# Kernel tuning notes

Hardware: AMD Instinct MI355X
Metric: run time of the kernel (lower is better)

The kernel has to match this reference:

```python
import jax, jax.numpy as jnp
import numpy as np

LN_EPS = 1e-5

def _layernorm(x, g, b):
    mu = jnp.mean(x, axis=-1, keepdims=True)
    var = jnp.mean(jnp.square(x - mu), axis=-1, keepdims=True)
    return (x - mu) * jax.lax.rsqrt(var + LN_EPS) * g + b

def setup_inputs() -> dict:
    key = jax.random.key(0)
    ks = jax.random.split(key, 8)
    B, T, C = 4, 2048, 1024
    s = 0.02
    return {
        "x": jax.random.normal(ks[0], (B, T, C), jnp.float32),
        "w_qkv": jax.random.normal(ks[1], (C, 3 * C), jnp.float32) * s,
        "b_qkv": jnp.zeros((3 * C,), jnp.float32),
        "w_out": jax.random.normal(ks[2], (C, C), jnp.float32) * s,
        "b_out": jnp.zeros((C,), jnp.float32),
        "w1": jax.random.normal(ks[3], (C, 4 * C), jnp.float32) * s,
        "b1": jnp.zeros((4 * C,), jnp.float32),
        "w2": jax.random.normal(ks[4], (4 * C, C), jnp.float32) * s,
        "b2": jnp.zeros((C,), jnp.float32),
        "g1": jnp.ones((C,), jnp.float32),
        "be1": jnp.zeros((C,), jnp.float32),
        "g2": jnp.ones((C,), jnp.float32),
        "be2": jnp.zeros((C,), jnp.float32),
        "n_head": 16,
    }

def reference(x, w_qkv, b_qkv, w_out, b_out, w1, b1, w2, b2, g1, be1, g2, be2, n_head):
    B, T, C = x.shape
    H = n_head
    D = C // H
    # --- causal self-attention ---
    qkv = x @ w_qkv + b_qkv                      # [B,T,3C]
    q, k, v = jnp.split(qkv, 3, axis=-1)
    q = q.reshape(B, T, H, D).transpose(0, 2, 1, 3)  # [B,H,T,D]
    k = k.reshape(B, T, H, D).transpose(0, 2, 1, 3)
    v = v.reshape(B, T, H, D).transpose(0, 2, 1, 3)
    attn = jnp.einsum("bhqd,bhkd->bhqk", q, k) * (1.0 / np.sqrt(D))
    causal = jnp.tril(jnp.ones((T, T), bool))
    attn = jnp.where(causal, attn, jnp.float32(-jnp.inf))
    attn = jax.nn.softmax(attn, axis=-1)
    y = jnp.einsum("bhqk,bhkd->bhqd", attn, v)
    y = y.transpose(0, 2, 1, 3).reshape(B, T, C)
    y = y @ w_out + b_out
    # post-norm residual (norm applied to sublayer output)
    x = x + _layernorm(y, g1, be1)
    # --- MLP ---
    h = jax.nn.gelu(x @ w1 + b1, approximate=False)
    h = h @ w2 + b2
    x = x + _layernorm(h, g2, be2)
    return x
```

## Files before the change

### kernel.cpp

```cpp
#include <hip/hip_runtime.h>
#include <hip/hip_bf16.h>

typedef unsigned short ushort_t;
using bf16x8 = __attribute__((ext_vector_type(8))) short;
using f32x4  = __attribute__((ext_vector_type(4))) float;

#define DEV __device__ __forceinline__

DEV unsigned short f2bf(float f) {
    unsigned int u = __builtin_bit_cast(unsigned int, f);
    u = (u + 0x7fffu + ((u >> 16) & 1u)) >> 16;
    return (unsigned short)u;
}

DEV int cvtpk_bf16(float lo, float hi) {
    int r;
    asm("v_cvt_pk_bf16_f32 %0, %1, %2" : "=v"(r) : "v"(lo), "v"(hi));
    return r;
}

DEV void gload16(const unsigned short* g, unsigned short* l) {
    __builtin_amdgcn_global_load_lds(
        (const __attribute__((address_space(1))) void*)g,
        (__attribute__((address_space(3))) void*)l, 16, 0, 0);
}

DEV float gelu_f(float v) {
    float u = v * (0.79788456f + 0.03567741f * v * v);
    float t = __builtin_amdgcn_exp2f(u * 2.88539008f);
    return v * t * __builtin_amdgcn_rcpf(t + 1.0f);
}

__global__ __launch_bounds__(256) void cvtbf_kernel(const float* __restrict__ in,
                                                    unsigned short* __restrict__ out) {
    int i = (blockIdx.x * 256 + threadIdx.x) * 4;
    float4 v = *(const float4*)&in[i];
    out[i + 0] = f2bf(v.x);
    out[i + 1] = f2bf(v.y);
    out[i + 2] = f2bf(v.z);
    out[i + 3] = f2bf(v.w);
}

__global__ __launch_bounds__(256) void transpose_cvt_kernel(const float* __restrict__ in,
                                                            unsigned short* __restrict__ out,
                                                            int R, int C) {
    __shared__ float t[32][33];
    int tx = threadIdx.x, ty = threadIdx.y;
    int c0 = blockIdx.x * 32, r0 = blockIdx.y * 32;
#pragma unroll
    for (int i = 0; i < 4; ++i)
        t[ty + i * 8][tx] = in[(size_t)(r0 + ty + i * 8) * C + c0 + tx];
    __syncthreads();
#pragma unroll
    for (int i = 0; i < 4; ++i)
        out[(size_t)(c0 + ty + i * 8) * R + r0 + tx] = f2bf(t[tx][ty + i * 8]);
}

__global__ __launch_bounds__(256) void vtrans_kernel(const unsigned short* __restrict__ qkvb,
                                                     unsigned short* __restrict__ vtg) {
    __shared__ unsigned short t[64 * 66];
    const int tid = threadIdx.x;
    const int t0 = blockIdx.x * 64;
    const int bh = blockIdx.y;
    const int b = bh >> 4, h = bh & 15;
    const unsigned short* src = qkvb + (size_t)(b * 2048 + t0) * 3072 + 2048 + h * 64;
#pragma unroll
    for (int c = 0; c < 2; ++c) {
        int cid = c * 256 + tid;
        int row = cid >> 3, cc = cid & 7;
        *(int4*)&t[row * 66 + cc * 8] = *(const int4*)&src[(size_t)row * 3072 + cc * 8];
    }
    __syncthreads();
    unsigned short* dst = vtg + (size_t)bh * 64 * 2048 + t0;
#pragma unroll
    for (int c = 0; c < 2; ++c) {
        int cid = c * 256 + tid;
        int d = cid >> 3, cc2 = cid & 7;
        bf16x8 v;
#pragma unroll
        for (int j = 0; j < 8; ++j) v[j] = (short)t[(cc2 * 8 + j) * 66 + d];
        *(bf16x8*)&dst[(size_t)d * 2048 + cc2 * 8] = v;
    }
}

template <int BM, int ACT, int OBF>
__global__ __launch_bounds__(512, 2) void gemm256_kernel(
    const unsigned short* __restrict__ A, const unsigned short* __restrict__ Bt,
    const float* __restrict__ bias, void* __restrict__ out,
    int N, int K, int gridNt) {
    constexpr int MF = BM / 32;
    constexpr int ALD = BM / 64;
    constexpr int NW = ALD / 2 + 2;
    constexpr int LB = (BM == 256) ? 8 : 7;
    __shared__ __align__(16) unsigned short lA[2][BM * 64];
    __shared__ __align__(16) unsigned short lB[2][256 * 64];
    const int tid = threadIdx.x;
    const int lane = tid & 63, wid = tid >> 6;
    const int g = lane >> 4, lr = lane & 15;
    const int wm = wid >> 2, wn = wid & 3;

    const int nwg = gridDim.x, cpx = nwg >> 3, bid = blockIdx.x;
    const int wkid = (bid & 7) * cpx + (bid >> 3);
    const int mt = wkid / gridNt, nt = wkid % gridNt;
    const int m0 = mt * BM, n0 = nt * 256;

    auto stageA = [&](int s, int kt, int bb) {
        int c = s * 512 + tid;
        int row = c & (BM - 1), kb = c >> LB;
        gload16(&A[(size_t)(m0 + row) * K + kt * 64 + kb * 8],
                &lA[bb][(size_t)(s * 512 + (tid & ~63)) * 8]);
    };
    auto stageB = [&](int s, int kt, int bb) {
        int c = s * 512 + tid;
        int row = c & 255, kb = c >> 8;
        gload16(&Bt[(size_t)(n0 + row) * K + kt * 64 + kb * 8],
                &lB[bb][(size_t)(s * 512 + (tid & ~63)) * 8]);
    };
    auto stageKh = [&](int half, int kt, int bb) {
        if constexpr (BM == 256) {
            stageA(half * 2 + 0, kt, bb);
            stageA(half * 2 + 1, kt, bb);
            stageB(half * 2 + 0, kt, bb);
            stageB(half * 2 + 1, kt, bb);
        } else {
            stageA(half, kt, bb);
            stageB(half * 2 + 0, kt, bb);
            stageB(half * 2 + 1, kt, bb);
        }
    };

    f32x4 acc[MF][4] = {};
    bf16x8 af[MF];
    bf16x8 bfr[4];

    const int nkt = K >> 6;
    stageKh(0, 0, 0);
    stageKh(1, 0, 0);

    for (int kt = 0; kt < nkt; ++kt) {
        const int b = kt & 1;
        const bool more = (kt + 1 < nkt);
#pragma unroll
        for (int ks = 0; ks < 2; ++ks) {
            if (ks == 1 && !more)
                asm volatile("s_waitcnt vmcnt(0)" ::: "memory");
            else if constexpr (BM == 256)
                asm volatile("s_waitcnt vmcnt(4)" ::: "memory");
            else
                asm volatile("s_waitcnt vmcnt(3)" ::: "memory");
            __builtin_amdgcn_s_barrier();
            asm volatile("" ::: "memory");
#pragma unroll
            for (int mf = 0; mf < MF; ++mf) {
                int c = (ks * 4 + g) * BM + wm * (BM / 2) + mf * 16 + lr;
                af[mf] = *(const bf16x8*)&lA[b][(size_t)c * 8];
            }
#pragma unroll
            for (int nf = 0; nf < 4; ++nf) {
                int c = (ks * 4 + g) * 256 + wn * 64 + nf * 16 + lr;
                bfr[nf] = *(const bf16x8*)&lB[b][(size_t)c * 8];
            }
            if (more) stageKh(ks, kt + 1, b ^ 1);
            __builtin_amdgcn_s_setprio(1);
#pragma unroll
            for (int mf = 0; mf < MF; ++mf)
#pragma unroll
                for (int nf = 0; nf < 4; ++nf)
                    acc[mf][nf] = __builtin_amdgcn_mfma_f32_16x16x32_bf16(
                        af[mf], bfr[nf], acc[mf][nf], 0, 0, 0);
            __builtin_amdgcn_s_setprio(0);
        }
    }

#pragma unroll
    for (int mf = 0; mf < MF; ++mf) {
#pragma unroll
        for (int nf = 0; nf < 4; ++nf) {
            int col = n0 + wn * 64 + nf * 16 + lr;
            float bv = bias[col];
#pragma unroll
            for (int r = 0; r < 4; ++r) {
                int row = m0 + wm * (BM / 2) + mf * 16 + g * 4 + r;
                float v = acc[mf][nf][r] + bv;
                if (ACT == 1) v = gelu_f(v);
                if (OBF)
                    ((unsigned short*)out)[(size_t)row * N + col] = f2bf(v);
                else
                    ((float*)out)[(size_t)row * N + col] = v;
            }
        }
    }
}

__global__ __launch_bounds__(256) void attn_kernel(const unsigned short* __restrict__ qkv,
                                                   const unsigned short* __restrict__ vtg,
                                                   unsigned short* __restrict__ y) {
    __shared__ unsigned short Kl[2][4096];
    __shared__ unsigned short Vl[2][4096];
    const int tid = threadIdx.x, lane = tid & 63, w = tid >> 6;
    const int g = lane >> 4, lr = lane & 15;
    const int p = blockIdx.x, h = blockIdx.y, b = blockIdx.z;
    const int bh = b * 16 + h;
    const size_t rs3 = 3072;
    const unsigned short* qbase = qkv + (size_t)b * 2048 * rs3 + h * 64;
    const unsigned short* kbase = qbase + 1024;
    const unsigned short* vbase = vtg + (size_t)bh * 64 * 2048;

    int ksoff[2], vsoff[2], ldoff[2];
#pragma unroll
    for (int c = 0; c < 2; ++c) {
        int row = w * 16 + c * 8 + (lane >> 3);
        int ccs = (lane & 7) ^ (row & 7) ^ (row >> 3);
        ksoff[c] = row * 3072 + ccs * 8;
        vsoff[c] = row * 2048 + ccs * 8;
        ldoff[c] = (w * 16 + c * 8) * 64;
    }

    const int idxP0 = 4 * (32 * (g & 1) + lr);
    const int idxP1 = idxP0 + 64;
    int idxA[4];
#pragma unroll
    for (int r = 0; r < 4; ++r) idxA[r] = 4 * (g * 20 + r);
    const bool ghigh = (g >> 1) != 0;
    const float qscale = 0.125f * 1.44269504089f;

    auto process = [&](int J) {
        const int q0w = J * 128 + w * 32;
        const int ktend = 2 * J + 2;
#pragma unroll
        for (int c = 0; c < 2; ++c) {
            gload16(&kbase[ksoff[c]], &Kl[0][ldoff[c]]);
            gload16(&vbase[vsoff[c]], &Vl[0][ldoff[c]]);
        }
        int qf[2][2][4];
#pragma unroll
        for (int sub = 0; sub < 2; ++sub)
#pragma unroll
            for (int f = 0; f < 2; ++f) {
                int4 v = *(const int4*)&qbase[(size_t)(q0w + sub * 16 + lr) * rs3 + f * 32 + g * 8];
                int vv[4] = {v.x, v.y, v.z, v.w};
#pragma unroll
                for (int i = 0; i < 4; ++i) {
                    unsigned int u = (unsigned int)vv[i];
                    float lo = __builtin_bit_cast(float, u << 16) * qscale;
                    float hi = __builtin_bit_cast(float, u & 0xffff0000u) * qscale;
                    qf[sub][f][i] = cvtpk_bf16(lo, hi);
                }
            }

        f32x4 O[2][4] = {};
        float m_[2] = {-3.0e38f, -3.0e38f}, l_[2] = {0.f, 0.f};

        int buf = 0;
        for (int kt = 0; kt < ktend; ++kt) {
            asm volatile("s_waitcnt vmcnt(0)" ::: "memory");
            __builtin_amdgcn_s_barrier();
            asm volatile("" ::: "memory");
            if (kt + 1 < ktend) {
#pragma unroll
                for (int c = 0; c < 2; ++c) {
                    gload16(&kbase[(size_t)(kt + 1) * 64 * 3072 + ksoff[c]], &Kl[buf ^ 1][ldoff[c]]);
                    gload16(&vbase[vsoff[c] + (kt + 1) * 64], &Vl[buf ^ 1][ldoff[c]]);
                }
            }
            const unsigned short* Kc = Kl[buf];
            const unsigned short* Vc = Vl[buf];

            const bool act0 = (kt * 64) <= (q0w + 15);
            const bool act1 = (kt * 64) <= (q0w + 31);

            f32x4 s0[4], s1[4];
#pragma unroll
            for (int st = 0; st < 4; ++st) {
                int rbase = (st * 16 + lr) * 64;
                int sw = (lr & 7) ^ (st * 2 + (lr >> 3));
                bf16x8 kf0 = *(const bf16x8*)&Kc[rbase + ((g ^ sw) * 8)];
                bf16x8 kf1 = *(const bf16x8*)&Kc[rbase + (((4 + g) ^ sw) * 8)];
                if (act0) {
                    f32x4 a = {};
                    a = __builtin_amdgcn_mfma_f32_16x16x32_bf16(kf0, *(const bf16x8*)&qf[0][0], a, 0, 0, 0);
                    a = __builtin_amdgcn_mfma_f32_16x16x32_bf16(kf1, *(const bf16x8*)&qf[0][1], a, 0, 0, 0);
                    s0[st] = a;
                }
                if (act1) {
                    f32x4 a = {};
                    a = __builtin_amdgcn_mfma_f32_16x16x32_bf16(kf0, *(const bf16x8*)&qf[1][0], a, 0, 0, 0);
                    a = __builtin_amdgcn_mfma_f32_16x16x32_bf16(kf1, *(const bf16x8*)&qf[1][1], a, 0, 0, 0);
                    s1[st] = a;
                }
            }

            int wt0[2][4], wt1[2][4];
#pragma unroll
            for (int sub = 0; sub < 2; ++sub) {
                if (sub == 0 && !act0) continue;
                if (sub == 1 && !act1) continue;
                f32x4* s = (sub == 0) ? s0 : s1;
                const int qmin = q0w + sub * 16;
                if (kt * 64 + 63 > qmin) {
                    int qv = qmin + lr;
#pragma unroll
                    for (int st = 0; st < 4; ++st) {
                        int keyb = kt * 64 + st * 16 + g * 4;
#pragma unroll
                        for (int r = 0; r < 4; ++r)
                            if (keyb + r > qv) s[st][r] = -3.0e38f;
                    }
                }
                float mx = fmaxf(fmaxf(s[0][0], s[0][1]), fmaxf(s[0][2], s[0][3]));
#pragma unroll
                for (int st = 1; st < 4; ++st)
                    mx = fmaxf(mx, fmaxf(fmaxf(s[st][0], s[st][1]), fmaxf(s[st][2], s[st][3])));
                mx = fmaxf(mx, __shfl_xor(mx, 16));
                mx = fmaxf(mx, __shfl_xor(mx, 32));
                float mold = m_[sub];
                float mnew = fmaxf(mold, mx);
                float alpha = __builtin_amdgcn_exp2f(mold - mnew);
                m_[sub] = mnew;
                float rs = 0.f;
#pragma unroll
                for (int st = 0; st < 4; ++st)
#pragma unroll
                    for (int r = 0; r < 4; ++r) {
                        float pp = __builtin_amdgcn_exp2f(s[st][r] - mnew);
                        s[st][r] = pp;
                        rs += pp;
                    }
                rs += __shfl_xor(rs, 16);
                rs += __shfl_xor(rs, 32);
                l_[sub] = l_[sub] * alpha + rs;
                int av = __builtin_bit_cast(int, alpha);
                f32x4* Os = O[sub];
#pragma unroll
                for (int r = 0; r < 4; ++r) {
                    float ar = __builtin_bit_cast(float, __builtin_amdgcn_ds_bpermute(idxA[r], av));
#pragma unroll
                    for (int dt = 0; dt < 4; ++dt) Os[dt][r] *= ar;
                }
                int ws_[4][2];
#pragma unroll
                for (int st = 0; st < 4; ++st) {
                    ws_[st][0] = cvtpk_bf16(s[st][0], s[st][1]);
                    ws_[st][1] = cvtpk_bf16(s[st][2], s[st][3]);
                }
                int(*wt)[4] = (sub == 0) ? wt0 : wt1;
#pragma unroll
                for (int ks = 0; ks < 2; ++ks)
#pragma unroll
                    for (int hp = 0; hp < 4; ++hp) {
                        int idx = (hp < 2) ? idxP0 : idxP1;
                        int v0 = __builtin_amdgcn_ds_bpermute(idx, ws_[2 * ks][hp & 1]);
                        int v1 = __builtin_amdgcn_ds_bpermute(idx, ws_[2 * ks + 1][hp & 1]);
                        wt[ks][hp] = ghigh ? v1 : v0;
                    }
            }

#pragma unroll
            for (int ks = 0; ks < 2; ++ks) {
                bf16x8 pa0 = *(const bf16x8*)&wt0[ks][0];
                bf16x8 pa1 = *(const bf16x8*)&wt1[ks][0];
#pragma unroll
                for (int dt = 0; dt < 4; ++dt) {
                    int d = dt * 16 + lr;
                    int xv = (ks * 4 + g) ^ (lr & 7) ^ (dt * 2 + (lr >> 3));
                    bf16x8 vf = *(const bf16x8*)&Vc[d * 64 + xv * 8];
                    if (act0) O[0][dt] = __builtin_amdgcn_mfma_f32_16x16x32_bf16(pa0, vf, O[0][dt], 0, 0, 0);
                    if (act1) O[1][dt] = __builtin_amdgcn_mfma_f32_16x16x32_bf16(pa1, vf, O[1][dt], 0, 0, 0);
                }
            }
            buf ^= 1;
        }

#pragma unroll
        for (int sub = 0; sub < 2; ++sub) {
            int lv = __builtin_bit_cast(int, l_[sub]);
#pragma unroll
            for (int r = 0; r < 4; ++r) {
                float lval = __builtin_bit_cast(float, __builtin_amdgcn_ds_bpermute(idxA[r], lv));
                float inv = __builtin_amdgcn_rcpf(lval);
                int q = q0w + sub * 16 + g * 4 + r;
#pragma unroll
                for (int dt = 0; dt < 4; ++dt)
                    y[(size_t)(b * 2048 + q) * 1024 + h * 64 + dt * 16 + lr] =
                        f2bf(O[sub][dt][r] * inv);
            }
        }
    };

    process(15 - p);
    __syncthreads();
    process(p);
}

template <int WRITE_BF>
__global__ __launch_bounds__(256) void ln_kernel(const float* __restrict__ base,
                                                 const float* __restrict__ delta,
                                                 const float* __restrict__ gw,
                                                 const float* __restrict__ bw,
                                                 float* __restrict__ outf,
                                                 unsigned short* __restrict__ outb) {
    const int row = blockIdx.x;
    const int tid = threadIdx.x;
    const float* d = delta + (size_t)row * 1024;
    const float* bs = base + (size_t)row * 1024;
    float4 x = *(const float4*)&d[tid * 4];
    float s = x.x + x.y + x.z + x.w;
    float s2 = x.x * x.x + x.y * x.y + x.z * x.z + x.w * x.w;
#pragma unroll
    for (int off = 1; off < 64; off <<= 1) {
        s += __shfl_xor(s, off);
        s2 += __shfl_xor(s2, off);
    }
    __shared__ float red[8];
    if ((tid & 63) == 0) {
        red[tid >> 6] = s;
        red[4 + (tid >> 6)] = s2;
    }
    __syncthreads();
    s = red[0] + red[1] + red[2] + red[3];
    s2 = red[4] + red[5] + red[6] + red[7];
    float mu = s * (1.f / 1024.f);
    float var = s2 * (1.f / 1024.f) - mu * mu;
    float rsig = rsqrtf(var + 1e-5f);
    float4 bb = *(const float4*)&bs[tid * 4];
    float4 gv = *(const float4*)&gw[tid * 4];
    float4 bv = *(const float4*)&bw[tid * 4];
    float4 o;
    o.x = bb.x + (x.x - mu) * rsig * gv.x + bv.x;
    o.y = bb.y + (x.y - mu) * rsig * gv.y + bv.y;
    o.z = bb.z + (x.z - mu) * rsig * gv.z + bv.z;
    o.w = bb.w + (x.w - mu) * rsig * gv.w + bv.w;
    *(float4*)&outf[(size_t)row * 1024 + tid * 4] = o;
    if (WRITE_BF) {
        unsigned short* ob = outb + (size_t)row * 1024 + tid * 4;
        ob[0] = f2bf(o.x);
        ob[1] = f2bf(o.y);
        ob[2] = f2bf(o.z);
        ob[3] = f2bf(o.w);
    }
}

extern "C" void kernel_launch(void* const* d_in, const int* in_sizes, int n_in,
                              void* d_out, int out_size, void* d_ws, size_t ws_size,
                              hipStream_t stream) {
    const float* x = (const float*)d_in[0];
    const float* w_qkv = (const float*)d_in[1];
    const float* b_qkv = (const float*)d_in[2];
    const float* w_out = (const float*)d_in[3];
    const float* b_out = (const float*)d_in[4];
    const float* w1 = (const float*)d_in[5];
    const float* b1 = (const float*)d_in[6];
    const float* w2 = (const float*)d_in[7];
    const float* b2 = (const float*)d_in[8];
    const float* g1 = (const float*)d_in[9];
    const float* be1 = (const float*)d_in[10];
    const float* g2 = (const float*)d_in[11];
    const float* be2 = (const float*)d_in[12];

    const size_t MB = 1ull << 20;
    if (ws_size < 184 * MB) return;
    char* ws = (char*)d_ws;
    unsigned short* xb    = (unsigned short*)(ws + 0);
    unsigned short* vtg   = (unsigned short*)(ws + 0);
    unsigned short* wqkvt = (unsigned short*)(ws + 16 * MB);
    unsigned short* qkvb  = (unsigned short*)(ws + 22 * MB);
    unsigned short* hb    = (unsigned short*)(ws + 0);
    unsigned short* woutt = (unsigned short*)(ws + 70 * MB);
    unsigned short* yb    = (unsigned short*)(ws + 72 * MB);
    float*          attnp = (float*)(ws + 88 * MB);
    float*          ff    = (float*)(ws + 88 * MB);
    float*          x2f   = (float*)(ws + 120 * MB);
    unsigned short* x2b   = (unsigned short*)(ws + 152 * MB);
    unsigned short* w1t   = (unsigned short*)(ws + 168 * MB);
    unsigned short* w2t   = (unsigned short*)(ws + 176 * MB);

    cvtbf_kernel<<<8192, 256, 0, stream>>>(x, xb);
    transpose_cvt_kernel<<<dim3(96, 32), dim3(32, 8), 0, stream>>>(w_qkv, wqkvt, 1024, 3072);
    transpose_cvt_kernel<<<dim3(32, 32), dim3(32, 8), 0, stream>>>(w_out, woutt, 1024, 1024);
    transpose_cvt_kernel<<<dim3(128, 32), dim3(32, 8), 0, stream>>>(w1, w1t, 1024, 4096);
    transpose_cvt_kernel<<<dim3(32, 128), dim3(32, 8), 0, stream>>>(w2, w2t, 4096, 1024);
    gemm256_kernel<256, 0, 1><<<384, 512, 0, stream>>>(xb, wqkvt, b_qkv, qkvb, 3072, 1024, 12);
    vtrans_kernel<<<dim3(32, 64), 256, 0, stream>>>(qkvb, vtg);
    attn_kernel<<<dim3(8, 16, 4), 256, 0, stream>>>(qkvb, vtg, yb);
    gemm256_kernel<128, 0, 0><<<256, 512, 0, stream>>>(yb, woutt, b_out, attnp, 1024, 1024, 4);
    ln_kernel<1><<<8192, 256, 0, stream>>>(x, attnp, g1, be1, x2f, x2b);
    gemm256_kernel<256, 1, 1><<<512, 512, 0, stream>>>(x2b, w1t, b1, hb, 4096, 1024, 16);
    gemm256_kernel<128, 0, 0><<<256, 512, 0, stream>>>(hb, w2t, b2, ff, 1024, 4096, 4);
    ln_kernel<0><<<8192, 256, 0, stream>>>(x2f, ff, g2, be2, (float*)d_out, nullptr);
}
```

Measured before the change: 511.6 us.

## Shrink GEMM tiles to 128x128 and widen attention KV tiles with lazy rescaling

Replaces the 256-wide, 512-thread GEMM with a single 128x128, 256-thread kernel and raises the grid sizes to match, so more workgroups are in flight but each one reuses less data. The attention kernel now loads 128-key K/V tiles, remaps blocks so heads are grouped per XCD, and drops the per-subtile causal activity checks. It also skips the online-softmax rescale unless the running max grows past a threshold. Larger tiles mean fewer loop iterations and barriers, but more wasted masked work on the diagonal and more register pressure.

```diff
diff --git a/kernel.cpp b/kernel.cpp
--- a/kernel.cpp
+++ b/kernel.cpp
@@ -83,87 +83,73 @@
     }
 }
 
-template <int BM, int ACT, int OBF>
-__global__ __launch_bounds__(512, 2) void gemm256_kernel(
+template <int ACT, int OBF>
+__global__ __launch_bounds__(256, 2) void gemm_kernel(
     const unsigned short* __restrict__ A, const unsigned short* __restrict__ Bt,
     const float* __restrict__ bias, void* __restrict__ out,
     int N, int K, int gridNt) {
-    constexpr int MF = BM / 32;
-    constexpr int ALD = BM / 64;
-    constexpr int NW = ALD / 2 + 2;
-    constexpr int LB = (BM == 256) ? 8 : 7;
-    __shared__ __align__(16) unsigned short lA[2][BM * 64];
-    __shared__ __align__(16) unsigned short lB[2][256 * 64];
+    __shared__ __align__(16) unsigned short lA[2][128 * 64];
+    __shared__ __align__(16) unsigned short lB[2][128 * 64];
     const int tid = threadIdx.x;
     const int lane = tid & 63, wid = tid >> 6;
     const int g = lane >> 4, lr = lane & 15;
-    const int wm = wid >> 2, wn = wid & 3;
+    const int wm = wid >> 1, wn = wid & 1;
 
     const int nwg = gridDim.x, cpx = nwg >> 3, bid = blockIdx.x;
     const int wkid = (bid & 7) * cpx + (bid >> 3);
     const int mt = wkid / gridNt, nt = wkid % gridNt;
-    const int m0 = mt * BM, n0 = nt * 256;
+    const int m0 = mt * 128, n0 = nt * 128;
 
     auto stageA = [&](int s, int kt, int bb) {
-        int c = s * 512 + tid;
-        int row = c & (BM - 1), kb = c >> LB;
+        int c = s * 256 + tid;
+        int row = c & 127, kb = c >> 7;
         gload16(&A[(size_t)(m0 + row) * K + kt * 64 + kb * 8],
-                &lA[bb][(size_t)(s * 512 + (tid & ~63)) * 8]);
+                &lA[bb][(size_t)(s * 256 + (tid & ~63)) * 8]);
     };
     auto stageB = [&](int s, int kt, int bb) {
-        int c = s * 512 + tid;
-        int row = c & 255, kb = c >> 8;
+        int c = s * 256 + tid;
+        int row = c & 127, kb = c >> 7;
         gload16(&Bt[(size_t)(n0 + row) * K + kt * 64 + kb * 8],
-                &lB[bb][(size_t)(s * 512 + (tid & ~63)) * 8]);
+                &lB[bb][(size_t)(s * 256 + (tid & ~63)) * 8]);
     };
-    auto stageKh = [&](int half, int kt, int bb) {
-        if constexpr (BM == 256) {
-            stageA(half * 2 + 0, kt, bb);
-            stageA(half * 2 + 1, kt, bb);
-            stageB(half * 2 + 0, kt, bb);
-            stageB(half * 2 + 1, kt, bb);
-        } else {
-            stageA(half, kt, bb);
-            stageB(half * 2 + 0, kt, bb);
-            stageB(half * 2 + 1, kt, bb);
-        }
-    };
-
-    f32x4 acc[MF][4] = {};
-    bf16x8 af[MF];
-    bf16x8 bfr[4];
-
+
+    f32x4 acc[4][4] = {};
     const int nkt = K >> 6;
-    stageKh(0, 0, 0);
-    stageKh(1, 0, 0);
+
+    stageA(0, 0, 0); stageA(1, 0, 0); stageB(0, 0, 0); stageB(1, 0, 0);
+    stageA(2, 0, 0); stageA(3, 0, 0); stageB(2, 0, 0); stageB(3, 0, 0);
 
     for (int kt = 0; kt < nkt; ++kt) {
-        const int b = kt & 1;
+        const int buf = kt & 1;
         const bool more = (kt + 1 < nkt);
 #pragma unroll
         for (int ks = 0; ks < 2; ++ks) {
             if (ks == 1 && !more)
                 asm volatile("s_waitcnt vmcnt(0)" ::: "memory");
-            else if constexpr (BM == 256)
+            else
                 asm volatile("s_waitcnt vmcnt(4)" ::: "memory");
-            else
-                asm volatile("s_waitcnt vmcnt(3)" ::: "memory");
             __builtin_amdgcn_s_barrier();
             asm volatile("" ::: "memory");
-#pragma unroll
-            for (int mf = 0; mf < MF; ++mf) {
-                int c = (ks * 4 + g) * BM + wm * (BM / 2) + mf * 16 + lr;
-                af[mf] = *(const bf16x8*)&lA[b][(size_t)c * 8];
+            bf16x8 af[4], bfr[4];
+#pragma unroll
+            for (int mf = 0; mf < 4; ++mf) {
+                int c = (ks * 4 + g) * 128 + wm * 64 + mf * 16 + lr;
+                af[mf] = *(const bf16x8*)&lA[buf][(size_t)c * 8];
             }
 #pragma unroll
             for (int nf = 0; nf < 4; ++nf) {
-                int c = (ks * 4 + g) * 256 + wn * 64 + nf * 16 + lr;
-                bfr[nf] = *(const bf16x8*)&lB[b][(size_t)c * 8];
-            }
-            if (more) stageKh(ks, kt + 1, b ^ 1);
+                int c = (ks * 4 + g) * 128 + wn * 64 + nf * 16 + lr;
+                bfr[nf] = *(const bf16x8*)&lB[buf][(size_t)c * 8];
+            }
+            if (more) {
+                if (ks == 0) { stageA(0, kt + 1, buf ^ 1); stageA(1, kt + 1, buf ^ 1);
+                               stageB(0, kt + 1, buf ^ 1); stageB(1, kt + 1, buf ^ 1); }
+                else         { stageA(2, kt + 1, buf ^ 1); stageA(3, kt + 1, buf ^ 1);
+                               stageB(2, kt + 1, buf ^ 1); stageB(3, kt + 1, buf ^ 1); }
+            }
             __builtin_amdgcn_s_setprio(1);
 #pragma unroll
-            for (int mf = 0; mf < MF; ++mf)
+            for (int mf = 0; mf < 4; ++mf)
 #pragma unroll
                 for (int nf = 0; nf < 4; ++nf)
                     acc[mf][nf] = __builtin_amdgcn_mfma_f32_16x16x32_bf16(
@@ -173,14 +159,14 @@
     }
 
 #pragma unroll
-    for (int mf = 0; mf < MF; ++mf) {
+    for (int mf = 0; mf < 4; ++mf) {
 #pragma unroll
         for (int nf = 0; nf < 4; ++nf) {
             int col = n0 + wn * 64 + nf * 16 + lr;
             float bv = bias[col];
 #pragma unroll
             for (int r = 0; r < 4; ++r) {
-                int row = m0 + wm * (BM / 2) + mf * 16 + g * 4 + r;
+                int row = m0 + wm * 64 + mf * 16 + g * 4 + r;
                 float v = acc[mf][nf][r] + bv;
                 if (ACT == 1) v = gelu_f(v);
                 if (OBF)
@@ -192,28 +178,32 @@
     }
 }
 
-__global__ __launch_bounds__(256) void attn_kernel(const unsigned short* __restrict__ qkv,
-                                                   const unsigned short* __restrict__ vtg,
-                                                   unsigned short* __restrict__ y) {
-    __shared__ unsigned short Kl[2][4096];
-    __shared__ unsigned short Vl[2][4096];
+__global__ __launch_bounds__(256, 2) void attn_kernel(const unsigned short* __restrict__ qkv,
+                                                      const unsigned short* __restrict__ vtg,
+                                                      unsigned short* __restrict__ y) {
+    __shared__ unsigned short Kl[2][128 * 64];
+    __shared__ unsigned short Vl[2][64 * 128];
     const int tid = threadIdx.x, lane = tid & 63, w = tid >> 6;
     const int g = lane >> 4, lr = lane & 15;
-    const int p = blockIdx.x, h = blockIdx.y, b = blockIdx.z;
-    const int bh = b * 16 + h;
+    const int id = blockIdx.x + 8 * (blockIdx.y + 16 * blockIdx.z);
+    const int xcd = id & 7, wrk = id >> 3;
+    const int bh = xcd * 8 + (wrk & 7);
+    const int p = wrk >> 3;
+    const int b = bh >> 4, h = bh & 15;
     const size_t rs3 = 3072;
     const unsigned short* qbase = qkv + (size_t)b * 2048 * rs3 + h * 64;
     const unsigned short* kbase = qbase + 1024;
     const unsigned short* vbase = vtg + (size_t)bh * 64 * 2048;
 
-    int ksoff[2], vsoff[2], ldoff[2];
-#pragma unroll
-    for (int c = 0; c < 2; ++c) {
-        int row = w * 16 + c * 8 + (lane >> 3);
-        int ccs = (lane & 7) ^ (row & 7) ^ (row >> 3);
-        ksoff[c] = row * 3072 + ccs * 8;
-        vsoff[c] = row * 2048 + ccs * 8;
-        ldoff[c] = (w * 16 + c * 8) * 64;
+    int ksoff[4], vsoff[4], ldoff[4];
+#pragma unroll
+    for (int c = 0; c < 4; ++c) {
+        int cid = c * 256 + tid;
+        int krow = cid >> 3, kcc = cid & 7;
+        ksoff[c] = krow * 3072 + (kcc ^ (krow & 7) ^ ((krow >> 3) & 7)) * 8;
+        int d = cid >> 4, tcs = cid & 15;
+        vsoff[c] = d * 2048 + (tcs ^ ((d & 7) ^ ((d >> 3) & 7))) * 8;
+        ldoff[c] = (c * 256 + (tid & ~63)) * 8;
     }
 
     const int idxP0 = 4 * (32 * (g & 1) + lr);
@@ -226,9 +216,9 @@
 
     auto process = [&](int J) {
         const int q0w = J * 128 + w * 32;
-        const int ktend = 2 * J + 2;
-#pragma unroll
-        for (int c = 0; c < 2; ++c) {
+        const int ktend = J + 1;
+#pragma unroll
+        for (int c = 0; c < 4; ++c) {
             gload16(&kbase[ksoff[c]], &Kl[0][ldoff[c]]);
             gload16(&vbase[vsoff[c]], &Vl[0][ldoff[c]]);
         }
@@ -258,50 +248,41 @@
             asm volatile("" ::: "memory");
             if (kt + 1 < ktend) {
 #pragma unroll
-                for (int c = 0; c < 2; ++c) {
-                    gload16(&kbase[(size_t)(kt + 1) * 64 * 3072 + ksoff[c]], &Kl[buf ^ 1][ldoff[c]]);
-                    gload16(&vbase[vsoff[c] + (kt + 1) * 64], &Vl[buf ^ 1][ldoff[c]]);
+                for (int c = 0; c < 4; ++c) {
+                    gload16(&kbase[(size_t)(kt + 1) * 128 * 3072 + ksoff[c]], &Kl[buf ^ 1][ldoff[c]]);
+                    gload16(&vbase[vsoff[c] + (kt + 1) * 128], &Vl[buf ^ 1][ldoff[c]]);
                 }
             }
             const unsigned short* Kc = Kl[buf];
             const unsigned short* Vc = Vl[buf];
 
-            const bool act0 = (kt * 64) <= (q0w + 15);
-            const bool act1 = (kt * 64) <= (q0w + 31);
-
-            f32x4 s0[4], s1[4];
-#pragma unroll
-            for (int st = 0; st < 4; ++st) {
+            f32x4 s0[8], s1[8];
+#pragma unroll
+            for (int st = 0; st < 8; ++st) {
                 int rbase = (st * 16 + lr) * 64;
-                int sw = (lr & 7) ^ (st * 2 + (lr >> 3));
+                int sw = (lr & 7) ^ ((st * 2 + (lr >> 3)) & 7);
                 bf16x8 kf0 = *(const bf16x8*)&Kc[rbase + ((g ^ sw) * 8)];
                 bf16x8 kf1 = *(const bf16x8*)&Kc[rbase + (((4 + g) ^ sw) * 8)];
-                if (act0) {
-                    f32x4 a = {};
-                    a = __builtin_amdgcn_mfma_f32_16x16x32_bf16(kf0, *(const bf16x8*)&qf[0][0], a, 0, 0, 0);
-                    a = __builtin_amdgcn_mfma_f32_16x16x32_bf16(kf1, *(const bf16x8*)&qf[0][1], a, 0, 0, 0);
-                    s0[st] = a;
-                }
-                if (act1) {
-                    f32x4 a = {};
-                    a = __builtin_amdgcn_mfma_f32_16x16x32_bf16(kf0, *(const bf16x8*)&qf[1][0], a, 0, 0, 0);
-                    a = __builtin_amdgcn_mfma_f32_16x16x32_bf16(kf1, *(const bf16x8*)&qf[1][1], a, 0, 0, 0);
-                    s1[st] = a;
-                }
-            }
-
-            int wt0[2][4], wt1[2][4];
+                f32x4 a = {};
+                a = __builtin_amdgcn_mfma_f32_16x16x32_bf16(kf0, *(const bf16x8*)&qf[0][0], a, 0, 0, 0);
+                a = __builtin_amdgcn_mfma_f32_16x16x32_bf16(kf1, *(const bf16x8*)&qf[0][1], a, 0, 0, 0);
+                s0[st] = a;
+                f32x4 c = {};
+                c = __builtin_amdgcn_mfma_f32_16x16x32_bf16(kf0, *(const bf16x8*)&qf[1][0], c, 0, 0, 0);
+                c = __builtin_amdgcn_mfma_f32_16x16x32_bf16(kf1, *(const bf16x8*)&qf[1][1], c, 0, 0, 0);
+                s1[st] = c;
+            }
+
+            int wt0[4][4], wt1[4][4];
 #pragma unroll
             for (int sub = 0; sub < 2; ++sub) {
-                if (sub == 0 && !act0) continue;
-                if (sub == 1 && !act1) continue;
                 f32x4* s = (sub == 0) ? s0 : s1;
                 const int qmin = q0w + sub * 16;
-                if (kt * 64 + 63 > qmin) {
+                if (kt == J) {
                     int qv = qmin + lr;
 #pragma unroll
-                    for (int st = 0; st < 4; ++st) {
-                        int keyb = kt * 64 + st * 16 + g * 4;
+                    for (int st = 0; st < 8; ++st) {
+                        int keyb = kt * 128 + st * 16 + g * 4;
 #pragma unroll
                         for (int r = 0; r < 4; ++r)
                             if (keyb + r > qv) s[st][r] = -3.0e38f;
@@ -309,43 +290,45 @@
                 }
                 float mx = fmaxf(fmaxf(s[0][0], s[0][1]), fmaxf(s[0][2], s[0][3]));
 #pragma unroll
-                for (int st = 1; st < 4; ++st)
+                for (int st = 1; st < 8; ++st)
                     mx = fmaxf(mx, fmaxf(fmaxf(s[st][0], s[st][1]), fmaxf(s[st][2], s[st][3])));
                 mx = fmaxf(mx, __shfl_xor(mx, 16));
                 mx = fmaxf(mx, __shfl_xor(mx, 32));
-                float mold = m_[sub];
-                float mnew = fmaxf(mold, mx);
-                float alpha = __builtin_amdgcn_exp2f(mold - mnew);
-                m_[sub] = mnew;
+                if (__any(mx - m_[sub] > 11.5f)) {
+                    float mnew = fmaxf(m_[sub], mx);
+                    float alpha = __builtin_amdgcn_exp2f(m_[sub] - mnew);
+                    m_[sub] = mnew;
+                    l_[sub] *= alpha;
+                    int av = __builtin_bit_cast(int, alpha);
+                    f32x4* Os = O[sub];
+#pragma unroll
+                    for (int r = 0; r < 4; ++r) {
+                        float ar = __builtin_bit_cast(float, __builtin_amdgcn_ds_bpermute(idxA[r], av));
+#pragma unroll
+                        for (int dt = 0; dt < 4; ++dt) Os[dt][r] *= ar;
+                    }
+                }
                 float rs = 0.f;
 #pragma unroll
-                for (int st = 0; st < 4; ++st)
+                for (int st = 0; st < 8; ++st)
 #pragma unroll
                     for (int r = 0; r < 4; ++r) {
-                        float pp = __builtin_amdgcn_exp2f(s[st][r] - mnew);
+                        float pp = __builtin_amdgcn_exp2f(s[st][r] - m_[sub]);
                         s[st][r] = pp;
                         rs += pp;
                     }
                 rs += __shfl_xor(rs, 16);
                 rs += __shfl_xor(rs, 32);
-                l_[sub] = l_[sub] * alpha + rs;
-                int av = __builtin_bit_cast(int, alpha);
-                f32x4* Os = O[sub];
-#pragma unroll
-                for (int r = 0; r < 4; ++r) {
-                    float ar = __builtin_bit_cast(float, __builtin_amdgcn_ds_bpermute(idxA[r], av));
-#pragma unroll
-                    for (int dt = 0; dt < 4; ++dt) Os[dt][r] *= ar;
-                }
-                int ws_[4][2];
-#pragma unroll
-                for (int st = 0; st < 4; ++st) {
+                l_[sub] += rs;
+                int ws_[8][2];
+#pragma unroll
+                for (int st = 0; st < 8; ++st) {
                     ws_[st][0] = cvtpk_bf16(s[st][0], s[st][1]);
                     ws_[st][1] = cvtpk_bf16(s[st][2], s[st][3]);
                 }
                 int(*wt)[4] = (sub == 0) ? wt0 : wt1;
 #pragma unroll
-                for (int ks = 0; ks < 2; ++ks)
+                for (int ks = 0; ks < 4; ++ks)
 #pragma unroll
                     for (int hp = 0; hp < 4; ++hp) {
                         int idx = (hp < 2) ? idxP0 : idxP1;
@@ -356,16 +339,16 @@
             }
 
 #pragma unroll
-            for (int ks = 0; ks < 2; ++ks) {
+            for (int ks = 0; ks < 4; ++ks) {
                 bf16x8 pa0 = *(const bf16x8*)&wt0[ks][0];
                 bf16x8 pa1 = *(const bf16x8*)&wt1[ks][0];
 #pragma unroll
                 for (int dt = 0; dt < 4; ++dt) {
                     int d = dt * 16 + lr;
-                    int xv = (ks * 4 + g) ^ (lr & 7) ^ (dt * 2 + (lr >> 3));
-                    bf16x8 vf = *(const bf16x8*)&Vc[d * 64 + xv * 8];
-                    if (act0) O[0][dt] = __builtin_amdgcn_mfma_f32_16x16x32_bf16(pa0, vf, O[0][dt], 0, 0, 0);
-                    if (act1) O[1][dt] = __builtin_amdgcn_mfma_f32_16x16x32_bf16(pa1, vf, O[1][dt], 0, 0, 0);
+                    int tc = (ks * 4 + g) ^ ((lr & 7) ^ ((dt * 2 + (lr >> 3)) & 7));
+                    bf16x8 vf = *(const bf16x8*)&Vc[d * 128 + tc * 8];
+                    O[0][dt] = __builtin_amdgcn_mfma_f32_16x16x32_bf16(pa0, vf, O[0][dt], 0, 0, 0);
+                    O[1][dt] = __builtin_amdgcn_mfma_f32_16x16x32_bf16(pa1, vf, O[1][dt], 0, 0, 0);
                 }
             }
             buf ^= 1;
@@ -479,12 +462,12 @@
     transpose_cvt_kernel<<<dim3(32, 32), dim3(32, 8), 0, stream>>>(w_out, woutt, 1024, 1024);
     transpose_cvt_kernel<<<dim3(128, 32), dim3(32, 8), 0, stream>>>(w1, w1t, 1024, 4096);
     transpose_cvt_kernel<<<dim3(32, 128), dim3(32, 8), 0, stream>>>(w2, w2t, 4096, 1024);
-    gemm256_kernel<256, 0, 1><<<384, 512, 0, stream>>>(xb, wqkvt, b_qkv, qkvb, 3072, 1024, 12);
+    gemm_kernel<0, 1><<<1536, 256, 0, stream>>>(xb, wqkvt, b_qkv, qkvb, 3072, 1024, 24);
     vtrans_kernel<<<dim3(32, 64), 256, 0, stream>>>(qkvb, vtg);
     attn_kernel<<<dim3(8, 16, 4), 256, 0, stream>>>(qkvb, vtg, yb);
-    gemm256_kernel<128, 0, 0><<<256, 512, 0, stream>>>(yb, woutt, b_out, attnp, 1024, 1024, 4);
+    gemm_kernel<0, 0><<<512, 256, 0, stream>>>(yb, woutt, b_out, attnp, 1024, 1024, 8);
     ln_kernel<1><<<8192, 256, 0, stream>>>(x, attnp, g1, be1, x2f, x2b);
-    gemm256_kernel<256, 1, 1><<<512, 512, 0, stream>>>(x2b, w1t, b1, hb, 4096, 1024, 16);
-    gemm256_kernel<128, 0, 0><<<256, 512, 0, stream>>>(hb, w2t, b2, ff, 1024, 4096, 4);
+    gemm_kernel<1, 1><<<2048, 256, 0, stream>>>(x2b, w1t, b1, hb, 4096, 1024, 32);
+    gemm_kernel<0, 0><<<512, 256, 0, stream>>>(hb, w2t, b2, ff, 1024, 4096, 8);
     ln_kernel<0><<<8192, 256, 0, stream>>>(x2f, ff, g2, be2, (float*)d_out, nullptr);
 }
```

Measured after the change: 577.7 us. 1.13x slower.
